# Performance work log

Hardware: AMD Instinct MI355X
Metric: run time of the kernel (lower is better)

## Reference

```python
import jax, jax.numpy as jnp
import numpy as np

N_NODES = 100000
N_EDGES = 1600000
N_GRAPHS = 2048
D = 128
H = 128
EPS = 1e-5


def gcn_conv(x, src, dst, W, b, n):
    # x: [N, Din], W: [Din, Dout]; GCN with added self-loops and symmetric norm
    xw = x @ W                                       # [N, Dout]
    deg = jnp.zeros((n,), x.dtype).at[dst].add(1.0) + 1.0  # deg of A+I (counted on dst)
    dinv = jax.lax.rsqrt(deg)                        # [N]
    norm = dinv[src] * dinv[dst]                     # [E]
    msg = xw[src] * norm[:, None]                    # [E, Dout] gather + scale
    agg = jax.ops.segment_sum(msg, dst, num_segments=n)
    agg = agg + xw * (dinv * dinv)[:, None]          # self-loop contribution
    return agg + b


def gru_step_h0(x, W_ih, W_hh, b_ih, b_hh):
    # single GRU step with h0 = 0 (PyTorch gate order r, z, n)
    h0 = jnp.zeros_like(x)
    gi = x @ W_ih.T + b_ih                           # [G, 3H]
    gh = h0 @ W_hh.T + b_hh                          # [G, 3H] (zeros + b_hh)
    ir, iz, inn = jnp.split(gi, 3, axis=-1)
    hr, hz, hn = jnp.split(gh, 3, axis=-1)
    r = jax.nn.sigmoid(ir + hr)
    z = jax.nn.sigmoid(iz + hz)
    n = jnp.tanh(inn + r * hn)
    return (1.0 - z) * n + z * h0


def setup_inputs() -> dict:
    key = jax.random.key(0)
    ks = jax.random.split(key, 10)
    x = jax.random.normal(ks[0], (N_NODES, D), jnp.float32)
    edge_index = jax.random.randint(ks[1], (2, N_EDGES), 0, N_NODES, jnp.int32)
    batch = jnp.sort(jax.random.randint(ks[2], (N_NODES,), 0, N_GRAPHS, jnp.int32))
    s = 1.0 / np.sqrt(H)
    return {
        "x": x,
        "edge_index": edge_index,
        "batch": batch,
        "W1": jax.random.normal(ks[3], (D, H), jnp.float32) * s,
        "b1": jnp.zeros((H,), jnp.float32),
        "W2": jax.random.normal(ks[4], (H, H), jnp.float32) * s,
        "b2": jnp.zeros((H,), jnp.float32),
        "W_ih": jax.random.normal(ks[5], (3 * H, H), jnp.float32) * s,
        "W_hh": jax.random.normal(ks[6], (3 * H, H), jnp.float32) * s,
        "b_ih": jnp.zeros((3 * H,), jnp.float32),
        "b_hh": jnp.zeros((3 * H,), jnp.float32),
        "W_lin": jax.random.normal(ks[7], (1, H), jnp.float32) * s,
        "b_lin": jnp.zeros((1,), jnp.float32),
    }


def reference(x, edge_index, batch, W1, b1, W2, b2, W_ih, W_hh, b_ih, b_hh, W_lin, b_lin):
    src, dst = edge_index[0], edge_index[1]
    n = x.shape[0]
    h = jax.nn.relu(gcn_conv(x, src, dst, W1, b1, n))
    h = gcn_conv(h, src, dst, W2, b2, n)
    # global_mean_pool over graph ids
    sums = jax.ops.segment_sum(h, batch, num_segments=N_GRAPHS)
    cnts = jax.ops.segment_sum(jnp.ones((n,), h.dtype), batch, num_segments=N_GRAPHS)
    g = sums / jnp.maximum(cnts, 1.0)[:, None]       # [G, H]
    # dropout p=0.5 in eval mode -> identity
    g = gru_step_h0(g, W_ih, W_hh, b_ih, b_hh)
    g = jax.nn.relu(g)
    mu = jnp.mean(g, axis=-1, keepdims=True)
    var = jnp.mean(jnp.square(g - mu), axis=-1, keepdims=True)
    g = (g - mu) * jax.lax.rsqrt(var + EPS)          # layer_norm, no affine
    return g @ W_lin.T + b_lin                       # [G, 1]
```

## Files before the change

kernel.cpp:

```cpp
#include <hip/hip_runtime.h>
#include <hip/hip_bf16.h>
#include <math.h>

#define DHID 128
#define SH 8
#define BIN_T 8192
#define CAPSH 13
#define SRC_SH 13

typedef __attribute__((ext_vector_type(8))) short bf16x8;
typedef __attribute__((ext_vector_type(4))) float f32x4;

__device__ __forceinline__ int atomAddI(int* p, int v) {
    return __hip_atomic_fetch_add(p, v, __ATOMIC_RELAXED, __HIP_MEMORY_SCOPE_AGENT);
}
__device__ __forceinline__ float bf_lo(unsigned u) { return __uint_as_float(u << 16); }
__device__ __forceinline__ float bf_hi(unsigned u) { return __uint_as_float(u & 0xffff0000u); }
__device__ __forceinline__ float bf_us(unsigned short u) { return __uint_as_float((unsigned)u << 16); }
__device__ __forceinline__ unsigned short bf16_1(float f) {
    unsigned u = __float_as_uint(f);
    u += 0x7fffu + ((u >> 16) & 1u);
    return (unsigned short)(u >> 16);
}
__device__ __forceinline__ unsigned pack_bf16x2(float a, float b) {
    unsigned ua = __float_as_uint(a);
    unsigned ub = __float_as_uint(b);
    ua = (ua + 0x7fffu + ((ua >> 16) & 1u)) >> 16;
    ub = (ub + 0x7fffu + ((ub >> 16) & 1u)) & 0xffff0000u;
    return ua | ub;
}

__global__ __launch_bounds__(256) void bin_edges(const int* __restrict__ src,
                                                 const int* __restrict__ dst,
                                                 int* __restrict__ bcur,
                                                 unsigned* __restrict__ staged,
                                                 const float* __restrict__ W1,
                                                 const float* __restrict__ W2,
                                                 const float* __restrict__ Wih,
                                                 unsigned short* __restrict__ Wt1,
                                                 unsigned short* __restrict__ Wt2,
                                                 unsigned short* __restrict__ Wihb,
                                                 int E, int NB, int nb_bin) {
    int t = threadIdx.x;
    if (blockIdx.x >= nb_bin) {
        int idx = (blockIdx.x - nb_bin) * 256 + t;
        if (idx < 16384) {
            int k = idx >> 7, n = idx & 127;
            Wt1[n * 128 + k] = bf16_1(W1[idx]);
        } else if (idx < 32768) {
            int j = idx - 16384;
            int k = j >> 7, n = j & 127;
            Wt2[n * 128 + k] = bf16_1(W2[j]);
        } else if (idx < 32768 + 49152) {
            int j = idx - 32768;
            Wihb[j] = bf16_1(Wih[j]);
        }
        return;
    }
    __shared__ int lh[512], lbase[512], lcur[512];
    int e0 = blockIdx.x * BIN_T;
    int eend = min(e0 + BIN_T, E);
    for (int i = t; i < NB; i += 256) { lh[i] = 0; lcur[i] = 0; }
    __syncthreads();
    for (int e = e0 + t; e < eend; e += 256)
        atomicAdd(&lh[dst[e] >> SH], 1);
    __syncthreads();
    for (int i = t; i < NB; i += 256)
        lbase[i] = lh[i] ? atomAddI(&bcur[i], lh[i]) : 0;
    __syncthreads();
    for (int e = e0 + t; e < eend; e += 256) {
        int d = dst[e];
        int b = d >> SH;
        int pos = lbase[b] + atomicAdd(&lcur[b], 1);
        staged[((size_t)b << CAPSH) + pos] =
            (unsigned)src[e] | ((unsigned)(d & ((1 << SH) - 1)) << 24);
    }
}

__global__ __launch_bounds__(256) void scatter_csr(const unsigned* __restrict__ staged,
                                                   const int* __restrict__ bcur,
                                                   int* __restrict__ off,
                                                   float* __restrict__ dinv,
                                                   int* __restrict__ rec,
                                                   int N, int E, int NB) {
    __shared__ int hist[4096];
    __shared__ int sh[256];
    int t = threadIdx.x;
    int b = blockIdx.x;
    int node0 = b << SH;

    int s0 = (t < b) ? bcur[t] : 0;
    int s1 = (256 + t < b) ? bcur[256 + t] : 0;
    int s = s0 + s1;
#pragma unroll
    for (int o = 1; o < 64; o <<= 1) s += __shfl_xor(s, o);
    if ((t & 63) == 0) sh[t >> 6] = s;
    __syncthreads();
    int base = sh[0] + sh[1] + sh[2] + sh[3];
    __syncthreads();

    for (int i = t; i < 4096; i += 256) hist[i] = 0;
    __syncthreads();
    int cnt_b = bcur[b];
    const unsigned* st = staged + ((size_t)b << CAPSH);
    for (int j = t; j < cnt_b; j += 256) {
        unsigned w = st[j];
        int key = (int)((w >> 24) << 4) | (int)((w & 0xFFFFFFu) >> SRC_SH);
        atomicAdd(&hist[key], 1);
    }
    __syncthreads();

    int loc[16];
    int run = 0;
    int base16 = t * 16;
#pragma unroll
    for (int i = 0; i < 16; i++) { loc[i] = run; run += hist[base16 + i]; }
    sh[t] = run;
    __syncthreads();
#pragma unroll
    for (int o = 1; o < 256; o <<= 1) {
        int x = (t >= o) ? sh[t - o] : 0;
        __syncthreads();
        sh[t] += x;
        __syncthreads();
    }
    int excl = sh[t] - run;
#pragma unroll
    for (int i = 0; i < 16; i++) hist[base16 + i] = base + excl + loc[i];

    int node = node0 + t;
    if (node < N) {
        off[node] = base + excl;
        dinv[node] = rsqrtf((float)run + 1.0f);
    }
    if (b == NB - 1 && t == 0) off[N] = E;
    __syncthreads();

    for (int j = t; j < cnt_b; j += 256) {
        unsigned w = st[j];
        int key = (int)((w >> 24) << 4) | (int)((w & 0xFFFFFFu) >> SRC_SH);
        int pos = atomicAdd(&hist[key], 1);
        rec[pos] = (int)(w & 0xFFFFFFu);
    }
}

__global__ __launch_bounds__(256) void gemm_mfma(const void* __restrict__ Xv,
                                                 const unsigned short* __restrict__ Wt,
                                                 unsigned short* __restrict__ Y,
                                                 int N, int x_is_bf16,
                                                 int wstride, int ystride) {
    __shared__ unsigned short Xs[64 * 136];
    __shared__ unsigned short Ws[128 * 136];
    const int tid = threadIdx.x;
    const unsigned short* Wg = Wt + (size_t)blockIdx.y * wstride;
    unsigned short* Yg = Y + (size_t)blockIdx.y * ystride;

    {
        const uint4* W4 = (const uint4*)Wg;
#pragma unroll
        for (int i = 0; i < 8; i++) {
            int idx = tid + i * 256;
            int r = idx >> 4, c8 = idx & 15;
            *(uint4*)&Ws[r * 136 + c8 * 8] = W4[idx];
        }
    }
    const int row0 = blockIdx.x * 64;
    if (x_is_bf16) {
        const uint4* X4 = (const uint4*)Xv;
#pragma unroll
        for (int i = 0; i < 4; i++) {
            int idx = tid + i * 256;
            int r = idx >> 4, c8 = idx & 15;
            uint4 v = make_uint4(0u, 0u, 0u, 0u);
            if (row0 + r < N) v = X4[(size_t)(row0 + r) * 16 + c8];
            *(uint4*)&Xs[r * 136 + c8 * 8] = v;
        }
    } else {
        const float4* X4 = (const float4*)Xv;
#pragma unroll
        for (int i = 0; i < 8; i++) {
            int idx = tid + i * 256;
            int r = idx >> 5, c4 = idx & 31;
            float4 v = make_float4(0.f, 0.f, 0.f, 0.f);
            if (row0 + r < N) v = X4[(size_t)(row0 + r) * 32 + c4];
            uint2 pk = make_uint2(pack_bf16x2(v.x, v.y), pack_bf16x2(v.z, v.w));
            *(uint2*)&Xs[r * 136 + c4 * 4] = pk;
        }
    }
    __syncthreads();

    const int lane = tid & 63;
    const int wv = tid >> 6;
    const int m = lane & 15, quad = lane >> 4;
    const int wrow = wv * 16;

    f32x4 acc[8];
#pragma unroll
    for (int i = 0; i < 8; i++) acc[i] = (f32x4){0.f, 0.f, 0.f, 0.f};

#pragma unroll
    for (int kc = 0; kc < 4; kc++) {
        bf16x8 a = *(const bf16x8*)&Xs[(wrow + m) * 136 + kc * 32 + quad * 8];
#pragma unroll
        for (int nt = 0; nt < 8; nt++) {
            bf16x8 b = *(const bf16x8*)&Ws[(nt * 16 + m) * 136 + kc * 32 + quad * 8];
            acc[nt] = __builtin_amdgcn_mfma_f32_16x16x32_bf16(a, b, acc[nt], 0, 0, 0);
        }
    }

#pragma unroll
    for (int r = 0; r < 4; r++) {
        int lrow = wrow + quad * 4 + r;
#pragma unroll
        for (int nt = 0; nt < 8; nt++)
            Xs[lrow * 136 + nt * 16 + m] = bf16_1(acc[nt][r]);
    }
    __syncthreads();
#pragma unroll
    for (int i = 0; i < 4; i++) {
        int idx = tid + i * 256;
        int r = idx >> 4, c8 = idx & 15;
        if (row0 + r < N)
            *(uint4*)&Yg[(size_t)(row0 + r) * DHID + c8 * 8] =
                *(const uint4*)&Xs[r * 136 + c8 * 8];
    }
}

__global__ __launch_bounds__(256) void aggregate(const unsigned short* __restrict__ A,
                                                 const float* __restrict__ dinv,
                                                 const int* __restrict__ off,
                                                 const int* __restrict__ rec,
                                                 const float* __restrict__ bias,
                                                 unsigned short* __restrict__ Bout,
                                                 int N, int mode) {
    int node = blockIdx.x * 4 + (threadIdx.x >> 6);
    if (node >= N) return;
    int lane = threadIdx.x & 63;
    int q  = lane >> 4;
    int ql = lane & 15;
    float di = dinv[node];
    float2 acc[4];
    if (q == 0) {
        float s = di * di;
        uint4 v = ((const uint4*)(A + (size_t)node * DHID))[ql];
        const float4* bb = (const float4*)(bias + ql * 8);
        float4 b0 = bb[0], b1 = bb[1];
        acc[0] = make_float2(bf_lo(v.x) * s + b0.x, bf_hi(v.x) * s + b0.y);
        acc[1] = make_float2(bf_lo(v.y) * s + b0.z, bf_hi(v.y) * s + b0.w);
        acc[2] = make_float2(bf_lo(v.z) * s + b1.x, bf_hi(v.z) * s + b1.y);
        acc[3] = make_float2(bf_lo(v.w) * s + b1.z, bf_hi(v.w) * s + b1.w);
    } else {
#pragma unroll
        for (int i = 0; i < 4; i++) acc[i] = make_float2(0.f, 0.f);
    }
    int j = off[node] + q;
    int jend = off[node + 1];
    if (j + 4 < jend) {
        int s0 = rec[j], s1 = rec[j + 4];
        for (; j + 12 < jend; j += 8) {
            int n0 = rec[j + 8], n1 = rec[j + 12];
            uint4 v0 = ((const uint4*)(A + (size_t)s0 * DHID))[ql];
            uint4 v1 = ((const uint4*)(A + (size_t)s1 * DHID))[ql];
            float w0 = dinv[s0] * di;
            float w1 = dinv[s1] * di;
            acc[0].x += bf_lo(v0.x) * w0 + bf_lo(v1.x) * w1;
            acc[0].y += bf_hi(v0.x) * w0 + bf_hi(v1.x) * w1;
            acc[1].x += bf_lo(v0.y) * w0 + bf_lo(v1.y) * w1;
            acc[1].y += bf_hi(v0.y) * w0 + bf_hi(v1.y) * w1;
            acc[2].x += bf_lo(v0.z) * w0 + bf_lo(v1.z) * w1;
            acc[2].y += bf_hi(v0.z) * w0 + bf_hi(v1.z) * w1;
            acc[3].x += bf_lo(v0.w) * w0 + bf_lo(v1.w) * w1;
            acc[3].y += bf_hi(v0.w) * w0 + bf_hi(v1.w) * w1;
            s0 = n0; s1 = n1;
        }
        {
            uint4 v0 = ((const uint4*)(A + (size_t)s0 * DHID))[ql];
            uint4 v1 = ((const uint4*)(A + (size_t)s1 * DHID))[ql];
            float w0 = dinv[s0] * di;
            float w1 = dinv[s1] * di;
            acc[0].x += bf_lo(v0.x) * w0 + bf_lo(v1.x) * w1;
            acc[0].y += bf_hi(v0.x) * w0 + bf_hi(v1.x) * w1;
            acc[1].x += bf_lo(v0.y) * w0 + bf_lo(v1.y) * w1;
            acc[1].y += bf_hi(v0.y) * w0 + bf_hi(v1.y) * w1;
            acc[2].x += bf_lo(v0.z) * w0 + bf_lo(v1.z) * w1;
            acc[2].y += bf_hi(v0.z) * w0 + bf_hi(v1.z) * w1;
            acc[3].x += bf_lo(v0.w) * w0 + bf_lo(v1.w) * w1;
            acc[3].y += bf_hi(v0.w) * w0 + bf_hi(v1.w) * w1;
            j += 8;
        }
    }
    if (j < jend) {
        int s0 = rec[j];
        uint4 v0 = ((const uint4*)(A + (size_t)s0 * DHID))[ql];
        float w0 = dinv[s0] * di;
        acc[0].x += bf_lo(v0.x) * w0;
        acc[0].y += bf_hi(v0.x) * w0;
        acc[1].x += bf_lo(v0.y) * w0;
        acc[1].y += bf_hi(v0.y) * w0;
        acc[2].x += bf_lo(v0.z) * w0;
        acc[2].y += bf_hi(v0.z) * w0;
        acc[3].x += bf_lo(v0.w) * w0;
        acc[3].y += bf_hi(v0.w) * w0;
    }
#pragma unroll
    for (int i = 0; i < 4; i++) {
        acc[i].x += __shfl_xor(acc[i].x, 16);
        acc[i].y += __shfl_xor(acc[i].y, 16);
        acc[i].x += __shfl_xor(acc[i].x, 32);
        acc[i].y += __shfl_xor(acc[i].y, 32);
    }
    if (q == 0) {
        if (mode == 1) {
#pragma unroll
            for (int i = 0; i < 4; i++) {
                acc[i].x = fmaxf(acc[i].x, 0.f);
                acc[i].y = fmaxf(acc[i].y, 0.f);
            }
        }
        uint4 pk;
        pk.x = pack_bf16x2(acc[0].x, acc[0].y);
        pk.y = pack_bf16x2(acc[1].x, acc[1].y);
        pk.z = pack_bf16x2(acc[2].x, acc[2].y);
        pk.w = pack_bf16x2(acc[3].x, acc[3].y);
        ((uint4*)(Bout + (size_t)node * DHID))[ql] = pk;
    }
}

__global__ __launch_bounds__(256) void pool_mean(const unsigned short* __restrict__ B,
                                                 const int* __restrict__ batch,
                                                 float* __restrict__ g, int N, int G) {
    __shared__ int se[2];
    __shared__ float red[128];
    const int t = threadIdx.x;
    const int gr = blockIdx.x;
    if (t < 2) {
        int target = gr + t, lo = 0, hi = N;
        while (lo < hi) {
            int mid = (lo + hi) >> 1;
            if (batch[mid] < target) lo = mid + 1; else hi = mid;
        }
        se[t] = lo;
    }
    __syncthreads();
    const int s = se[0], e = se[1];
    const int col = t & 127, rh = t >> 7;
    float sum = 0.f;
    for (int r = s + rh; r < e; r += 2) sum += bf_us(B[(size_t)r * DHID + col]);
    if (rh == 1) red[col] = sum;
    __syncthreads();
    if (rh == 0) {
        float tot = sum + red[col];
        g[(size_t)gr * DHID + col] = tot / fmaxf((float)(e - s), 1.0f);
    }
}

__global__ __launch_bounds__(128) void gate_ln_head(const unsigned short* __restrict__ gi,
                                                    const float* __restrict__ b_ih,
                                                    const float* __restrict__ b_hh,
                                                    const float* __restrict__ W_lin,
                                                    const float* __restrict__ b_lin,
                                                    float* __restrict__ out, int G) {
    __shared__ float red[2];
    const int t = threadIdx.x;
    const int g = blockIdx.x;

    float d0 = bf_us(gi[(size_t)g * DHID + t]);
    float d1 = bf_us(gi[(size_t)(G + g) * DHID + t]);
    float d2 = bf_us(gi[(size_t)(2 * G + g) * DHID + t]);

    float rg = 1.f / (1.f + expf(-(d0 + b_ih[t] + b_hh[t])));
    float zg = 1.f / (1.f + expf(-(d1 + b_ih[128 + t] + b_hh[128 + t])));
    float ng = tanhf(d2 + b_ih[256 + t] + rg * b_hh[256 + t]);
    float y = fmaxf((1.f - zg) * ng, 0.f);

    auto blockSum = [&](float v) -> float {
#pragma unroll
        for (int o = 1; o < 64; o <<= 1) v += __shfl_xor(v, o);
        __syncthreads();
        if ((t & 63) == 0) red[t >> 6] = v;
        __syncthreads();
        return red[0] + red[1];
    };

    float mu = blockSum(y) * (1.f / 128.f);
    float dy = y - mu;
    float var = blockSum(dy * dy) * (1.f / 128.f);
    float yn = dy * rsqrtf(var + 1e-5f);
    float tot = blockSum(yn * W_lin[t]);
    if (t == 0) out[g] = tot + b_lin[0];
}

extern "C" void kernel_launch(void* const* d_in, const int* in_sizes, int n_in,
                              void* d_out, int out_size, void* d_ws, size_t ws_size,
                              hipStream_t stream) {
    const float* x     = (const float*)d_in[0];
    const int*   ei    = (const int*)d_in[1];
    const int*   batch = (const int*)d_in[2];
    const float* W1    = (const float*)d_in[3];
    const float* b1    = (const float*)d_in[4];
    const float* W2    = (const float*)d_in[5];
    const float* b2    = (const float*)d_in[6];
    const float* W_ih  = (const float*)d_in[7];
    const float* b_ih  = (const float*)d_in[9];
    const float* b_hh  = (const float*)d_in[10];
    const float* W_lin = (const float*)d_in[11];
    const float* b_lin = (const float*)d_in[12];
    float* out = (float*)d_out;

    const int N = in_sizes[0] / DHID;
    const int E = in_sizes[1] / 2;
    const int G = out_size;
    const int* src = ei;
    const int* dst = ei + E;
    const int NB = (N + (1 << SH) - 1) >> SH;

    auto align256 = [](size_t v) { return (v + 255) & ~(size_t)255; };
    char* p = (char*)d_ws;
    size_t used = 0;
    auto carve = [&](size_t bytes) -> char* {
        char* q = p + used;
        used += align256(bytes);
        return q;
    };

    int*   off    = (int*)carve(((size_t)N + 1) * 4);
    int*   bcur   = (int*)carve(512 * 4);
    float* dinv   = (float*)carve((size_t)N * 4);
    unsigned* staged = (unsigned*)carve(((size_t)NB << CAPSH) * 4);
    int*   rec    = (int*)carve((size_t)E * 4);
    float* gbuf   = (float*)carve((size_t)G * DHID * 4);
    unsigned short* Wt1  = (unsigned short*)carve((size_t)128 * 128 * 2);
    unsigned short* Wt2  = (unsigned short*)carve((size_t)128 * 128 * 2);
    unsigned short* Wihb = (unsigned short*)carve((size_t)3 * 128 * 128 * 2);
    unsigned short* gib  = (unsigned short*)carve((size_t)3 * G * DHID * 2);
    unsigned short* A    = (unsigned short*)carve((size_t)N * DHID * 2);
    unsigned short* B1b  = (unsigned short*)carve((size_t)N * DHID * 2);
    size_t matB = (size_t)N * DHID * 2;
    unsigned short* B2b;
    if (ws_size >= used + matB) {
        B2b = (unsigned short*)carve(matB);
    } else {
        B2b = (unsigned short*)d_in[0];
    }

    dim3 blk(256);
    int nb_g  = (N + 63) / 64;
    int nb_ag = (N + 3) / 4;
    int nb_bin = (E + BIN_T - 1) / BIN_T;
    int nb_wp  = (81920 + 255) / 256;

    hipMemsetAsync(bcur, 0, (size_t)NB * 4, stream);
    bin_edges<<<nb_bin + nb_wp, blk, 0, stream>>>(src, dst, bcur, staged,
                                                  W1, W2, W_ih, Wt1, Wt2, Wihb,
                                                  E, NB, nb_bin);
    scatter_csr<<<NB, blk, 0, stream>>>(staged, bcur, off, dinv, rec, N, E, NB);

    gemm_mfma<<<dim3(nb_g, 1), blk, 0, stream>>>(x, Wt1, A, N, 0, 0, 0);
    aggregate<<<nb_ag, blk, 0, stream>>>(A, dinv, off, rec, b1, B1b, N, 1);

    gemm_mfma<<<dim3(nb_g, 1), blk, 0, stream>>>(B1b, Wt2, A, N, 1, 0, 0);
    aggregate<<<nb_ag, blk, 0, stream>>>(A, dinv, off, rec, b2, B2b, N, 0);

    pool_mean<<<G, blk, 0, stream>>>(B2b, batch, gbuf, N, G);
    gemm_mfma<<<dim3((G + 63) / 64, 3), blk, 0, stream>>>(gbuf, Wihb, gib, G, 0,
                                                          128 * 128, G * DHID);
    gate_ln_head<<<G, dim3(128), 0, stream>>>(gib, b_ih, b_hh, W_lin, b_lin, out, G);
}
```

Before: 348.7 us.

## Fuse CSR scatter with first GEMM, aggregation with GEMM, and aggregation with pooling

Runs the CSR scatter and the first feature GEMM in the same launch as separate block ranges. It fuses the layer-1 aggregation with the layer-2 GEMM, and fuses the layer-2 aggregation with mean pooling through per-block segmented sums and atomic adds into a zeroed pool buffer. Per-graph inverse counts are now computed in the binning kernel. This removes several launches and the round trips of intermediate N×128 matrices through global memory. In exchange it adds float atomics, which make the pooled sums order-dependent, and an extra bf16 rounding of the scaled values before pooling.

Result: no change. 355.5 us (+2.0%).

```diff
diff --git a/kernel.cpp b/kernel.cpp
--- a/kernel.cpp
+++ b/kernel.cpp
@@ -30,216 +30,13 @@
     return ua | ub;
 }
 
-__global__ __launch_bounds__(256) void bin_edges(const int* __restrict__ src,
-                                                 const int* __restrict__ dst,
-                                                 int* __restrict__ bcur,
-                                                 unsigned* __restrict__ staged,
-                                                 const float* __restrict__ W1,
-                                                 const float* __restrict__ W2,
-                                                 const float* __restrict__ Wih,
-                                                 unsigned short* __restrict__ Wt1,
-                                                 unsigned short* __restrict__ Wt2,
-                                                 unsigned short* __restrict__ Wihb,
-                                                 int E, int NB, int nb_bin) {
-    int t = threadIdx.x;
-    if (blockIdx.x >= nb_bin) {
-        int idx = (blockIdx.x - nb_bin) * 256 + t;
-        if (idx < 16384) {
-            int k = idx >> 7, n = idx & 127;
-            Wt1[n * 128 + k] = bf16_1(W1[idx]);
-        } else if (idx < 32768) {
-            int j = idx - 16384;
-            int k = j >> 7, n = j & 127;
-            Wt2[n * 128 + k] = bf16_1(W2[j]);
-        } else if (idx < 32768 + 49152) {
-            int j = idx - 32768;
-            Wihb[j] = bf16_1(Wih[j]);
-        }
-        return;
-    }
-    __shared__ int lh[512], lbase[512], lcur[512];
-    int e0 = blockIdx.x * BIN_T;
-    int eend = min(e0 + BIN_T, E);
-    for (int i = t; i < NB; i += 256) { lh[i] = 0; lcur[i] = 0; }
-    __syncthreads();
-    for (int e = e0 + t; e < eend; e += 256)
-        atomicAdd(&lh[dst[e] >> SH], 1);
-    __syncthreads();
-    for (int i = t; i < NB; i += 256)
-        lbase[i] = lh[i] ? atomAddI(&bcur[i], lh[i]) : 0;
-    __syncthreads();
-    for (int e = e0 + t; e < eend; e += 256) {
-        int d = dst[e];
-        int b = d >> SH;
-        int pos = lbase[b] + atomicAdd(&lcur[b], 1);
-        staged[((size_t)b << CAPSH) + pos] =
-            (unsigned)src[e] | ((unsigned)(d & ((1 << SH) - 1)) << 24);
-    }
-}
-
-__global__ __launch_bounds__(256) void scatter_csr(const unsigned* __restrict__ staged,
-                                                   const int* __restrict__ bcur,
-                                                   int* __restrict__ off,
-                                                   float* __restrict__ dinv,
-                                                   int* __restrict__ rec,
-                                                   int N, int E, int NB) {
-    __shared__ int hist[4096];
-    __shared__ int sh[256];
-    int t = threadIdx.x;
-    int b = blockIdx.x;
-    int node0 = b << SH;
-
-    int s0 = (t < b) ? bcur[t] : 0;
-    int s1 = (256 + t < b) ? bcur[256 + t] : 0;
-    int s = s0 + s1;
-#pragma unroll
-    for (int o = 1; o < 64; o <<= 1) s += __shfl_xor(s, o);
-    if ((t & 63) == 0) sh[t >> 6] = s;
-    __syncthreads();
-    int base = sh[0] + sh[1] + sh[2] + sh[3];
-    __syncthreads();
-
-    for (int i = t; i < 4096; i += 256) hist[i] = 0;
-    __syncthreads();
-    int cnt_b = bcur[b];
-    const unsigned* st = staged + ((size_t)b << CAPSH);
-    for (int j = t; j < cnt_b; j += 256) {
-        unsigned w = st[j];
-        int key = (int)((w >> 24) << 4) | (int)((w & 0xFFFFFFu) >> SRC_SH);
-        atomicAdd(&hist[key], 1);
-    }
-    __syncthreads();
-
-    int loc[16];
-    int run = 0;
-    int base16 = t * 16;
-#pragma unroll
-    for (int i = 0; i < 16; i++) { loc[i] = run; run += hist[base16 + i]; }
-    sh[t] = run;
-    __syncthreads();
-#pragma unroll
-    for (int o = 1; o < 256; o <<= 1) {
-        int x = (t >= o) ? sh[t - o] : 0;
-        __syncthreads();
-        sh[t] += x;
-        __syncthreads();
-    }
-    int excl = sh[t] - run;
-#pragma unroll
-    for (int i = 0; i < 16; i++) hist[base16 + i] = base + excl + loc[i];
-
-    int node = node0 + t;
-    if (node < N) {
-        off[node] = base + excl;
-        dinv[node] = rsqrtf((float)run + 1.0f);
-    }
-    if (b == NB - 1 && t == 0) off[N] = E;
-    __syncthreads();
-
-    for (int j = t; j < cnt_b; j += 256) {
-        unsigned w = st[j];
-        int key = (int)((w >> 24) << 4) | (int)((w & 0xFFFFFFu) >> SRC_SH);
-        int pos = atomicAdd(&hist[key], 1);
-        rec[pos] = (int)(w & 0xFFFFFFu);
-    }
-}
-
-__global__ __launch_bounds__(256) void gemm_mfma(const void* __restrict__ Xv,
-                                                 const unsigned short* __restrict__ Wt,
-                                                 unsigned short* __restrict__ Y,
-                                                 int N, int x_is_bf16,
-                                                 int wstride, int ystride) {
-    __shared__ unsigned short Xs[64 * 136];
-    __shared__ unsigned short Ws[128 * 136];
-    const int tid = threadIdx.x;
-    const unsigned short* Wg = Wt + (size_t)blockIdx.y * wstride;
-    unsigned short* Yg = Y + (size_t)blockIdx.y * ystride;
-
-    {
-        const uint4* W4 = (const uint4*)Wg;
-#pragma unroll
-        for (int i = 0; i < 8; i++) {
-            int idx = tid + i * 256;
-            int r = idx >> 4, c8 = idx & 15;
-            *(uint4*)&Ws[r * 136 + c8 * 8] = W4[idx];
-        }
-    }
-    const int row0 = blockIdx.x * 64;
-    if (x_is_bf16) {
-        const uint4* X4 = (const uint4*)Xv;
-#pragma unroll
-        for (int i = 0; i < 4; i++) {
-            int idx = tid + i * 256;
-            int r = idx >> 4, c8 = idx & 15;
-            uint4 v = make_uint4(0u, 0u, 0u, 0u);
-            if (row0 + r < N) v = X4[(size_t)(row0 + r) * 16 + c8];
-            *(uint4*)&Xs[r * 136 + c8 * 8] = v;
-        }
-    } else {
-        const float4* X4 = (const float4*)Xv;
-#pragma unroll
-        for (int i = 0; i < 8; i++) {
-            int idx = tid + i * 256;
-            int r = idx >> 5, c4 = idx & 31;
-            float4 v = make_float4(0.f, 0.f, 0.f, 0.f);
-            if (row0 + r < N) v = X4[(size_t)(row0 + r) * 32 + c4];
-            uint2 pk = make_uint2(pack_bf16x2(v.x, v.y), pack_bf16x2(v.z, v.w));
-            *(uint2*)&Xs[r * 136 + c4 * 4] = pk;
-        }
-    }
-    __syncthreads();
-
-    const int lane = tid & 63;
-    const int wv = tid >> 6;
-    const int m = lane & 15, quad = lane >> 4;
-    const int wrow = wv * 16;
-
-    f32x4 acc[8];
-#pragma unroll
-    for (int i = 0; i < 8; i++) acc[i] = (f32x4){0.f, 0.f, 0.f, 0.f};
-
-#pragma unroll
-    for (int kc = 0; kc < 4; kc++) {
-        bf16x8 a = *(const bf16x8*)&Xs[(wrow + m) * 136 + kc * 32 + quad * 8];
-#pragma unroll
-        for (int nt = 0; nt < 8; nt++) {
-            bf16x8 b = *(const bf16x8*)&Ws[(nt * 16 + m) * 136 + kc * 32 + quad * 8];
-            acc[nt] = __builtin_amdgcn_mfma_f32_16x16x32_bf16(a, b, acc[nt], 0, 0, 0);
-        }
-    }
-
-#pragma unroll
-    for (int r = 0; r < 4; r++) {
-        int lrow = wrow + quad * 4 + r;
-#pragma unroll
-        for (int nt = 0; nt < 8; nt++)
-            Xs[lrow * 136 + nt * 16 + m] = bf16_1(acc[nt][r]);
-    }
-    __syncthreads();
-#pragma unroll
-    for (int i = 0; i < 4; i++) {
-        int idx = tid + i * 256;
-        int r = idx >> 4, c8 = idx & 15;
-        if (row0 + r < N)
-            *(uint4*)&Yg[(size_t)(row0 + r) * DHID + c8 * 8] =
-                *(const uint4*)&Xs[r * 136 + c8 * 8];
-    }
-}
-
-__global__ __launch_bounds__(256) void aggregate(const unsigned short* __restrict__ A,
-                                                 const float* __restrict__ dinv,
-                                                 const int* __restrict__ off,
-                                                 const int* __restrict__ rec,
-                                                 const float* __restrict__ bias,
-                                                 unsigned short* __restrict__ Bout,
-                                                 int N, int mode) {
-    int node = blockIdx.x * 4 + (threadIdx.x >> 6);
-    if (node >= N) return;
-    int lane = threadIdx.x & 63;
-    int q  = lane >> 4;
-    int ql = lane & 15;
+__device__ __forceinline__ void gather_acc(const unsigned short* __restrict__ A,
+                                           const float* __restrict__ dinv,
+                                           const int* __restrict__ off,
+                                           const int* __restrict__ rec,
+                                           const float* __restrict__ bias,
+                                           int node, int q, int ql, float2 acc[4]) {
     float di = dinv[node];
-    float2 acc[4];
     if (q == 0) {
         float s = di * di;
         uint4 v = ((const uint4*)(A + (size_t)node * DHID))[ql];
@@ -309,48 +106,398 @@
         acc[i].x += __shfl_xor(acc[i].x, 32);
         acc[i].y += __shfl_xor(acc[i].y, 32);
     }
-    if (q == 0) {
-        if (mode == 1) {
-#pragma unroll
-            for (int i = 0; i < 4; i++) {
-                acc[i].x = fmaxf(acc[i].x, 0.f);
-                acc[i].y = fmaxf(acc[i].y, 0.f);
+}
+
+__global__ __launch_bounds__(256) void bin_edges(const int* __restrict__ src,
+                                                 const int* __restrict__ dst,
+                                                 int* __restrict__ bcur,
+                                                 unsigned* __restrict__ staged,
+                                                 const float* __restrict__ W1,
+                                                 const float* __restrict__ W2,
+                                                 const float* __restrict__ Wih,
+                                                 unsigned short* __restrict__ Wt1,
+                                                 unsigned short* __restrict__ Wt2,
+                                                 unsigned short* __restrict__ Wihb,
+                                                 const int* __restrict__ batch,
+                                                 float* __restrict__ cnt_inv,
+                                                 int E, int NB, int nb_bin, int Nn, int G) {
+    int t = threadIdx.x;
+    if (blockIdx.x >= nb_bin) {
+        int idx = (blockIdx.x - nb_bin) * 256 + t;
+        if (idx < 16384) {
+            int k = idx >> 7, n = idx & 127;
+            Wt1[n * 128 + k] = bf16_1(W1[idx]);
+        } else if (idx < 32768) {
+            int j = idx - 16384;
+            int k = j >> 7, n = j & 127;
+            Wt2[n * 128 + k] = bf16_1(W2[j]);
+        } else if (idx < 32768 + 49152) {
+            int j = idx - 32768;
+            Wihb[j] = bf16_1(Wih[j]);
+        } else if (idx < 81920 + G) {
+            int g = idx - 81920;
+            int lo = 0, hi = Nn;
+            while (lo < hi) { int mid = (lo + hi) >> 1; if (batch[mid] < g) lo = mid + 1; else hi = mid; }
+            int s = lo;
+            hi = Nn;
+            while (lo < hi) { int mid = (lo + hi) >> 1; if (batch[mid] < g + 1) lo = mid + 1; else hi = mid; }
+            cnt_inv[g] = 1.0f / fmaxf((float)(lo - s), 1.0f);
+        }
+        return;
+    }
+    __shared__ int lh[512], lbase[512], lcur[512];
+    int e0 = blockIdx.x * BIN_T;
+    int eend = min(e0 + BIN_T, E);
+    for (int i = t; i < NB; i += 256) { lh[i] = 0; lcur[i] = 0; }
+    __syncthreads();
+    for (int e = e0 + t; e < eend; e += 256)
+        atomicAdd(&lh[dst[e] >> SH], 1);
+    __syncthreads();
+    for (int i = t; i < NB; i += 256)
+        lbase[i] = lh[i] ? atomAddI(&bcur[i], lh[i]) : 0;
+    __syncthreads();
+    for (int e = e0 + t; e < eend; e += 256) {
+        int d = dst[e];
+        int b = d >> SH;
+        int pos = lbase[b] + atomicAdd(&lcur[b], 1);
+        staged[((size_t)b << CAPSH) + pos] =
+            (unsigned)src[e] | ((unsigned)(d & ((1 << SH) - 1)) << 24);
+    }
+}
+
+__global__ __launch_bounds__(256) void scatter_gemm(const unsigned* __restrict__ staged,
+                                                    const int* __restrict__ bcur,
+                                                    int* __restrict__ off,
+                                                    float* __restrict__ dinv,
+                                                    int* __restrict__ rec,
+                                                    int N, int E, int NB,
+                                                    const float* __restrict__ Xf,
+                                                    const unsigned short* __restrict__ Wt,
+                                                    unsigned short* __restrict__ Y) {
+    __shared__ __align__(16) unsigned char smem[52224];
+    const int tid = threadIdx.x;
+    if (blockIdx.x < NB) {
+        int* hist = (int*)smem;
+        int* sh   = (int*)(smem + 16384);
+        int t = tid;
+        int b = blockIdx.x;
+        int node0 = b << SH;
+
+        int s0 = (t < b) ? bcur[t] : 0;
+        int s1 = (256 + t < b) ? bcur[256 + t] : 0;
+        int s = s0 + s1;
+#pragma unroll
+        for (int o = 1; o < 64; o <<= 1) s += __shfl_xor(s, o);
+        if ((t & 63) == 0) sh[t >> 6] = s;
+        __syncthreads();
+        int base = sh[0] + sh[1] + sh[2] + sh[3];
+        __syncthreads();
+
+        for (int i = t; i < 4096; i += 256) hist[i] = 0;
+        __syncthreads();
+        int cnt_b = bcur[b];
+        const unsigned* st = staged + ((size_t)b << CAPSH);
+        for (int j = t; j < cnt_b; j += 256) {
+            unsigned w = st[j];
+            int key = (int)((w >> 24) << 4) | (int)((w & 0xFFFFFFu) >> SRC_SH);
+            atomicAdd(&hist[key], 1);
+        }
+        __syncthreads();
+
+        int loc[16];
+        int run = 0;
+        int base16 = t * 16;
+#pragma unroll
+        for (int i = 0; i < 16; i++) { loc[i] = run; run += hist[base16 + i]; }
+        sh[t] = run;
+        __syncthreads();
+#pragma unroll
+        for (int o = 1; o < 256; o <<= 1) {
+            int x = (t >= o) ? sh[t - o] : 0;
+            __syncthreads();
+            sh[t] += x;
+            __syncthreads();
+        }
+        int excl = sh[t] - run;
+#pragma unroll
+        for (int i = 0; i < 16; i++) hist[base16 + i] = base + excl + loc[i];
+
+        int node = node0 + t;
+        if (node < N) {
+            off[node] = base + excl;
+            dinv[node] = rsqrtf((float)run + 1.0f);
+        }
+        if (b == NB - 1 && t == 0) off[N] = E;
+        __syncthreads();
+
+        for (int j = t; j < cnt_b; j += 256) {
+            unsigned w = st[j];
+            int key = (int)((w >> 24) << 4) | (int)((w & 0xFFFFFFu) >> SRC_SH);
+            int pos = atomicAdd(&hist[key], 1);
+            rec[pos] = (int)(w & 0xFFFFFFu);
+        }
+    } else {
+        unsigned short* Xs = (unsigned short*)smem;
+        unsigned short* Ws = (unsigned short*)(smem + 17408);
+        {
+            const uint4* W4 = (const uint4*)Wt;
+#pragma unroll
+            for (int i = 0; i < 8; i++) {
+                int idx = tid + i * 256;
+                int r = idx >> 4, c8 = idx & 15;
+                *(uint4*)&Ws[r * 136 + c8 * 8] = W4[idx];
             }
         }
-        uint4 pk;
-        pk.x = pack_bf16x2(acc[0].x, acc[0].y);
-        pk.y = pack_bf16x2(acc[1].x, acc[1].y);
-        pk.z = pack_bf16x2(acc[2].x, acc[2].y);
-        pk.w = pack_bf16x2(acc[3].x, acc[3].y);
-        ((uint4*)(Bout + (size_t)node * DHID))[ql] = pk;
-    }
-}
-
-__global__ __launch_bounds__(256) void pool_mean(const unsigned short* __restrict__ B,
-                                                 const int* __restrict__ batch,
-                                                 float* __restrict__ g, int N, int G) {
-    __shared__ int se[2];
-    __shared__ float red[128];
-    const int t = threadIdx.x;
-    const int gr = blockIdx.x;
-    if (t < 2) {
-        int target = gr + t, lo = 0, hi = N;
-        while (lo < hi) {
-            int mid = (lo + hi) >> 1;
-            if (batch[mid] < target) lo = mid + 1; else hi = mid;
-        }
-        se[t] = lo;
-    }
-    __syncthreads();
-    const int s = se[0], e = se[1];
-    const int col = t & 127, rh = t >> 7;
+        const int row0 = (blockIdx.x - NB) * 64;
+        {
+            const float4* X4 = (const float4*)Xf;
+#pragma unroll
+            for (int i = 0; i < 8; i++) {
+                int idx = tid + i * 256;
+                int r = idx >> 5, c4 = idx & 31;
+                float4 v = make_float4(0.f, 0.f, 0.f, 0.f);
+                if (row0 + r < N) v = X4[(size_t)(row0 + r) * 32 + c4];
+                uint2 pk = make_uint2(pack_bf16x2(v.x, v.y), pack_bf16x2(v.z, v.w));
+                *(uint2*)&Xs[r * 136 + c4 * 4] = pk;
+            }
+        }
+        __syncthreads();
+
+        const int lane = tid & 63;
+        const int wv = tid >> 6;
+        const int m = lane & 15, quad = lane >> 4;
+        const int wrow = wv * 16;
+
+        f32x4 acc[8];
+#pragma unroll
+        for (int i = 0; i < 8; i++) acc[i] = (f32x4){0.f, 0.f, 0.f, 0.f};
+
+#pragma unroll
+        for (int kc = 0; kc < 4; kc++) {
+            bf16x8 a = *(const bf16x8*)&Xs[(wrow + m) * 136 + kc * 32 + quad * 8];
+#pragma unroll
+            for (int nt = 0; nt < 8; nt++) {
+                bf16x8 bfr = *(const bf16x8*)&Ws[(nt * 16 + m) * 136 + kc * 32 + quad * 8];
+                acc[nt] = __builtin_amdgcn_mfma_f32_16x16x32_bf16(a, bfr, acc[nt], 0, 0, 0);
+            }
+        }
+
+#pragma unroll
+        for (int r = 0; r < 4; r++) {
+            int lrow = wrow + quad * 4 + r;
+#pragma unroll
+            for (int nt = 0; nt < 8; nt++)
+                Xs[lrow * 136 + nt * 16 + m] = bf16_1(acc[nt][r]);
+        }
+        __syncthreads();
+#pragma unroll
+        for (int i = 0; i < 4; i++) {
+            int idx = tid + i * 256;
+            int r = idx >> 4, c8 = idx & 15;
+            if (row0 + r < N)
+                *(uint4*)&Y[(size_t)(row0 + r) * DHID + c8 * 8] =
+                    *(const uint4*)&Xs[r * 136 + c8 * 8];
+        }
+    }
+}
+
+__global__ __launch_bounds__(256) void agg_gemm(const unsigned short* __restrict__ A,
+                                                const float* __restrict__ dinv,
+                                                const int* __restrict__ off,
+                                                const int* __restrict__ rec,
+                                                const float* __restrict__ bias,
+                                                const unsigned short* __restrict__ Wt2,
+                                                unsigned short* __restrict__ Y,
+                                                int N) {
+    __shared__ unsigned short Xs[64 * 136];
+    const int tid = threadIdx.x;
+    const int lane = tid & 63;
+    const int wv = tid >> 6;
+    const int q = lane >> 4, ql = lane & 15;
+    const int row0 = blockIdx.x * 64;
+
+    for (int it = 0; it < 16; ++it) {
+        int node = row0 + wv * 16 + it;
+        int lr = wv * 16 + it;
+        if (node < N) {
+            float2 acc[4];
+            gather_acc(A, dinv, off, rec, bias, node, q, ql, acc);
+            if (q == 0) {
+                uint4 pk;
+                pk.x = pack_bf16x2(fmaxf(acc[0].x, 0.f), fmaxf(acc[0].y, 0.f));
+                pk.y = pack_bf16x2(fmaxf(acc[1].x, 0.f), fmaxf(acc[1].y, 0.f));
+                pk.z = pack_bf16x2(fmaxf(acc[2].x, 0.f), fmaxf(acc[2].y, 0.f));
+                pk.w = pack_bf16x2(fmaxf(acc[3].x, 0.f), fmaxf(acc[3].y, 0.f));
+                *(uint4*)&Xs[lr * 136 + ql * 8] = pk;
+            }
+        } else if (q == 0) {
+            *(uint4*)&Xs[lr * 136 + ql * 8] = make_uint4(0u, 0u, 0u, 0u);
+        }
+    }
+    const int m = lane & 15, quad = lane >> 4;
+    const int wrow = wv * 16;
+    f32x4 acc2[8];
+#pragma unroll
+    for (int i = 0; i < 8; i++) acc2[i] = (f32x4){0.f, 0.f, 0.f, 0.f};
+#pragma unroll
+    for (int kc = 0; kc < 4; kc++) {
+        bf16x8 a = *(const bf16x8*)&Xs[(wrow + m) * 136 + kc * 32 + quad * 8];
+#pragma unroll
+        for (int nt = 0; nt < 8; nt++) {
+            bf16x8 bfr = *(const bf16x8*)(Wt2 + (nt * 16 + m) * 128 + kc * 32 + quad * 8);
+            acc2[nt] = __builtin_amdgcn_mfma_f32_16x16x32_bf16(a, bfr, acc2[nt], 0, 0, 0);
+        }
+    }
+#pragma unroll
+    for (int r = 0; r < 4; r++) {
+        int lrow = wrow + quad * 4 + r;
+#pragma unroll
+        for (int nt = 0; nt < 8; nt++)
+            Xs[lrow * 136 + nt * 16 + m] = bf16_1(acc2[nt][r]);
+    }
+    __syncthreads();
+#pragma unroll
+    for (int i = 0; i < 4; i++) {
+        int idx = tid + i * 256;
+        int r = idx >> 4, c8 = idx & 15;
+        if (row0 + r < N)
+            *(uint4*)&Y[(size_t)(row0 + r) * DHID + c8 * 8] =
+                *(const uint4*)&Xs[r * 136 + c8 * 8];
+    }
+}
+
+__global__ __launch_bounds__(256) void agg_pool(const unsigned short* __restrict__ A,
+                                                const float* __restrict__ dinv,
+                                                const int* __restrict__ off,
+                                                const int* __restrict__ rec,
+                                                const float* __restrict__ bias,
+                                                const float* __restrict__ cnt_inv,
+                                                const int* __restrict__ batch,
+                                                float* __restrict__ gbuf,
+                                                int N) {
+    __shared__ unsigned short Xh[64 * 136];
+    __shared__ int sb[64];
+    const int tid = threadIdx.x;
+    const int row0 = blockIdx.x * 64;
+    if (tid < 64) sb[tid] = (row0 + tid < N) ? batch[row0 + tid] : -1;
+    __syncthreads();
+    const int lane = tid & 63;
+    const int wv = tid >> 6;
+    const int q = lane >> 4, ql = lane & 15;
+
+    for (int it = 0; it < 16; ++it) {
+        int node = row0 + wv * 16 + it;
+        int lr = wv * 16 + it;
+        if (node < N) {
+            float2 acc[4];
+            gather_acc(A, dinv, off, rec, bias, node, q, ql, acc);
+            if (q == 0) {
+                float sc = cnt_inv[sb[lr]];
+                uint4 pk;
+                pk.x = pack_bf16x2(acc[0].x * sc, acc[0].y * sc);
+                pk.y = pack_bf16x2(acc[1].x * sc, acc[1].y * sc);
+                pk.z = pack_bf16x2(acc[2].x * sc, acc[2].y * sc);
+                pk.w = pack_bf16x2(acc[3].x * sc, acc[3].y * sc);
+                *(uint4*)&Xh[lr * 136 + ql * 8] = pk;
+            }
+        }
+    }
+    __syncthreads();
+    const int col = tid & 127;
+    const int half = tid >> 7;
     float sum = 0.f;
-    for (int r = s + rh; r < e; r += 2) sum += bf_us(B[(size_t)r * DHID + col]);
-    if (rh == 1) red[col] = sum;
-    __syncthreads();
-    if (rh == 0) {
-        float tot = sum + red[col];
-        g[(size_t)gr * DHID + col] = tot / fmaxf((float)(e - s), 1.0f);
+    int cg = -1;
+    for (int r = half * 32; r < half * 32 + 32; ++r) {
+        int g = sb[r];
+        if (g != cg) {
+            if (cg >= 0) atomicAdd(&gbuf[(size_t)cg * DHID + col], sum);
+            sum = 0.f;
+            cg = g;
+        }
+        if (g >= 0) sum += bf_us(Xh[r * 136 + col]);
+    }
+    if (cg >= 0) atomicAdd(&gbuf[(size_t)cg * DHID + col], sum);
+}
+
+__global__ __launch_bounds__(256) void gemm_mfma(const void* __restrict__ Xv,
+                                                 const unsigned short* __restrict__ Wt,
+                                                 unsigned short* __restrict__ Y,
+                                                 int N, int x_is_bf16,
+                                                 int wstride, int ystride) {
+    __shared__ unsigned short Xs[64 * 136];
+    __shared__ unsigned short Ws[128 * 136];
+    const int tid = threadIdx.x;
+    const unsigned short* Wg = Wt + (size_t)blockIdx.y * wstride;
+    unsigned short* Yg = Y + (size_t)blockIdx.y * ystride;
+
+    {
+        const uint4* W4 = (const uint4*)Wg;
+#pragma unroll
+        for (int i = 0; i < 8; i++) {
+            int idx = tid + i * 256;
+            int r = idx >> 4, c8 = idx & 15;
+            *(uint4*)&Ws[r * 136 + c8 * 8] = W4[idx];
+        }
+    }
+    const int row0 = blockIdx.x * 64;
+    if (x_is_bf16) {
+        const uint4* X4 = (const uint4*)Xv;
+#pragma unroll
+        for (int i = 0; i < 4; i++) {
+            int idx = tid + i * 256;
+            int r = idx >> 4, c8 = idx & 15;
+            uint4 v = make_uint4(0u, 0u, 0u, 0u);
+            if (row0 + r < N) v = X4[(size_t)(row0 + r) * 16 + c8];
+            *(uint4*)&Xs[r * 136 + c8 * 8] = v;
+        }
+    } else {
+        const float4* X4 = (const float4*)Xv;
+#pragma unroll
+        for (int i = 0; i < 8; i++) {
+            int idx = tid + i * 256;
+            int r = idx >> 5, c4 = idx & 31;
+            float4 v = make_float4(0.f, 0.f, 0.f, 0.f);
+            if (row0 + r < N) v = X4[(size_t)(row0 + r) * 32 + c4];
+            uint2 pk = make_uint2(pack_bf16x2(v.x, v.y), pack_bf16x2(v.z, v.w));
+            *(uint2*)&Xs[r * 136 + c4 * 4] = pk;
+        }
+    }
+    __syncthreads();
+
+    const int lane = tid & 63;
+    const int wv = tid >> 6;
+    const int m = lane & 15, quad = lane >> 4;
+    const int wrow = wv * 16;
+
+    f32x4 acc[8];
+#pragma unroll
+    for (int i = 0; i < 8; i++) acc[i] = (f32x4){0.f, 0.f, 0.f, 0.f};
+
+#pragma unroll
+    for (int kc = 0; kc < 4; kc++) {
+        bf16x8 a = *(const bf16x8*)&Xs[(wrow + m) * 136 + kc * 32 + quad * 8];
+#pragma unroll
+        for (int nt = 0; nt < 8; nt++) {
+            bf16x8 b = *(const bf16x8*)&Ws[(nt * 16 + m) * 136 + kc * 32 + quad * 8];
+            acc[nt] = __builtin_amdgcn_mfma_f32_16x16x32_bf16(a, b, acc[nt], 0, 0, 0);
+        }
+    }
+
+#pragma unroll
+    for (int r = 0; r < 4; r++) {
+        int lrow = wrow + quad * 4 + r;
+#pragma unroll
+        for (int nt = 0; nt < 8; nt++)
+            Xs[lrow * 136 + nt * 16 + m] = bf16_1(acc[nt][r]);
+    }
+    __syncthreads();
+#pragma unroll
+    for (int i = 0; i < 4; i++) {
+        int idx = tid + i * 256;
+        int r = idx >> 4, c8 = idx & 15;
+        if (row0 + r < N)
+            *(uint4*)&Yg[(size_t)(row0 + r) * DHID + c8 * 8] =
+                *(const uint4*)&Xs[r * 136 + c8 * 8];
     }
 }
 
@@ -425,43 +572,35 @@
 
     int*   off    = (int*)carve(((size_t)N + 1) * 4);
     int*   bcur   = (int*)carve(512 * 4);
+    float* gbuf   = (float*)carve((size_t)G * DHID * 4);
     float* dinv   = (float*)carve((size_t)N * 4);
+    float* cnt_inv = (float*)carve((size_t)G * 4);
     unsigned* staged = (unsigned*)carve(((size_t)NB << CAPSH) * 4);
     int*   rec    = (int*)carve((size_t)E * 4);
-    float* gbuf   = (float*)carve((size_t)G * DHID * 4);
     unsigned short* Wt1  = (unsigned short*)carve((size_t)128 * 128 * 2);
     unsigned short* Wt2  = (unsigned short*)carve((size_t)128 * 128 * 2);
     unsigned short* Wihb = (unsigned short*)carve((size_t)3 * 128 * 128 * 2);
     unsigned short* gib  = (unsigned short*)carve((size_t)3 * G * DHID * 2);
     unsigned short* A    = (unsigned short*)carve((size_t)N * DHID * 2);
     unsigned short* B1b  = (unsigned short*)carve((size_t)N * DHID * 2);
-    size_t matB = (size_t)N * DHID * 2;
-    unsigned short* B2b;
-    if (ws_size >= used + matB) {
-        B2b = (unsigned short*)carve(matB);
-    } else {
-        B2b = (unsigned short*)d_in[0];
-    }
 
     dim3 blk(256);
     int nb_g  = (N + 63) / 64;
-    int nb_ag = (N + 3) / 4;
     int nb_bin = (E + BIN_T - 1) / BIN_T;
-    int nb_wp  = (81920 + 255) / 256;
-
-    hipMemsetAsync(bcur, 0, (size_t)NB * 4, stream);
+    int nb_wp  = (81920 + G + 255) / 256;
+
+    hipMemsetAsync(bcur, 0, 512 * 4 + (size_t)G * DHID * 4, stream);
     bin_edges<<<nb_bin + nb_wp, blk, 0, stream>>>(src, dst, bcur, staged,
                                                   W1, W2, W_ih, Wt1, Wt2, Wihb,
-                                                  E, NB, nb_bin);
-    scatter_csr<<<NB, blk, 0, stream>>>(staged, bcur, off, dinv, rec, N, E, NB);
-
-    gemm_mfma<<<dim3(nb_g, 1), blk, 0, stream>>>(x, Wt1, A, N, 0, 0, 0);
-    aggregate<<<nb_ag, blk, 0, stream>>>(A, dinv, off, rec, b1, B1b, N, 1);
-
-    gemm_mfma<<<dim3(nb_g, 1), blk, 0, stream>>>(B1b, Wt2, A, N, 1, 0, 0);
-    aggregate<<<nb_ag, blk, 0, stream>>>(A, dinv, off, rec, b2, B2b, N, 0);
-
-    pool_mean<<<G, blk, 0, stream>>>(B2b, batch, gbuf, N, G);
+                                                  batch, cnt_inv,
+                                                  E, NB, nb_bin, N, G);
+    scatter_gemm<<<NB + nb_g, blk, 0, stream>>>(staged, bcur, off, dinv, rec,
+                                                N, E, NB, x, Wt1, A);
+
+    agg_gemm<<<nb_g, blk, 0, stream>>>(A, dinv, off, rec, b1, Wt2, B1b, N);
+
+    agg_pool<<<nb_g, blk, 0, stream>>>(B1b, dinv, off, rec, b2, cnt_inv, batch, gbuf, N);
+
     gemm_mfma<<<dim3((G + 63) / 64, 3), blk, 0, stream>>>(gbuf, Wihb, gib, G, 0,
                                                           128 * 128, G * DHID);
     gate_ln_head<<<G, dim3(128), 0, stream>>>(gib, b_ih, b_hh, W_lin, b_lin, out, G);
```
